# Kernel tuning notes

Hardware: AMD Instinct MI355X
Metric: run time of the kernel (lower is better)

## Reference

```python
import jax, jax.numpy as jnp
import numpy as np

NEG = -1e6  # masked_softmax fill value from the original code


def setup_inputs() -> dict:
    key = jax.random.key(0)
    ks = jax.random.split(key, 8)
    B, Q, K, Dq, Dk, Dv, H = 8, 256, 1024, 256, 256, 128, 128
    queries = jax.random.normal(ks[0], (B, Q, Dq), dtype=jnp.float32)
    keys = jax.random.normal(ks[1], (B, K, Dk), dtype=jnp.float32)
    values = jax.random.normal(ks[2], (B, K, Dv), dtype=jnp.float32)
    valid_lens = jax.random.randint(ks[3], (B,), 1, K + 1, dtype=jnp.int32)
    # learned params (Dense, use_bias=False): y = x @ W
    W_q = jax.random.normal(ks[4], (Dq, H), dtype=jnp.float32) / np.sqrt(Dq)
    W_k = jax.random.normal(ks[5], (Dk, H), dtype=jnp.float32) / np.sqrt(Dk)
    w_v = jax.random.normal(ks[6], (H,), dtype=jnp.float32) / np.sqrt(H)
    return {"queries": queries, "keys": keys, "values": values,
            "valid_lens": valid_lens, "W_q": W_q, "W_k": W_k, "w_v": w_v}


def reference(queries, keys, values, valid_lens, W_q, W_k, w_v):
    q = jnp.einsum('bqd,dh->bqh', queries, W_q)          # [B,Q,H]
    k = jnp.einsum('bkd,dh->bkh', keys, W_k)             # [B,K,H]
    features = jnp.tanh(q[:, :, None, :] + k[:, None, :, :])  # [B,Q,K,H]
    scores = jnp.einsum('bqkh,h->bqk', features, w_v)    # [B,Q,K]
    # masked softmax over last axis: positions >= valid_len set to -1e6
    K_len = scores.shape[-1]
    mask = jnp.arange(K_len)[None, None, :] < valid_lens[:, None, None]
    scores = jnp.where(mask, scores, NEG)
    attn = jax.nn.softmax(scores, axis=-1)
    return jnp.einsum('bqk,bkv->bqv', attn, values)      # [B,Q,Dv]
```

## Files before the change

kernel.cpp:

```cpp
#include <hip/hip_runtime.h>
#include <hip/hip_bf16.h>

#if defined(__has_builtin)
#if __has_builtin(__builtin_amdgcn_exp2f)
#define EXP2F __builtin_amdgcn_exp2f
#endif
#if __has_builtin(__builtin_amdgcn_rcpf)
#define RCPF __builtin_amdgcn_rcpf
#endif
#endif
#ifndef EXP2F
#define EXP2F exp2f
#endif
#ifndef RCPF
#define RCPF(x) (1.0f / (x))
#endif

#define B_  8
#define Q_  256
#define K_  1024
#define D_  256
#define H_  128
#define DV_ 128

#define CSL 2.8853900817779268f
#define L2E 1.4426950408889634f

__global__ __launch_bounds__(256) void proj_kernel(
    const float* __restrict__ queries, const float* __restrict__ keys,
    const float* __restrict__ Wq, const float* __restrict__ Wk,
    float* __restrict__ qE, float* __restrict__ kE)
{
    __shared__ __align__(16) float As[16][36];
    __shared__ __align__(16) float Ws[32][128];

    const int tid = threadIdx.x;
    const int blk = blockIdx.x;
    const bool isQ = blk < 128;
    const int row0 = isQ ? blk * 16 : (blk - 128) * 16;
    const float* A = isQ ? (queries + row0 * D_) : (keys + row0 * D_);
    const float* W = isQ ? Wq : Wk;

    float acc[8];
#pragma unroll
    for (int j = 0; j < 8; j++) acc[j] = 0.f;

    const int r  = tid >> 4;
    const int c8 = (tid & 15) * 8;

    for (int d0 = 0; d0 < D_; d0 += 32) {
        if (tid < 128) {
            const int rr = tid >> 3, cc = (tid & 7) * 4;
            *(float4*)&As[rr][cc] = *(const float4*)&A[rr * D_ + d0 + cc];
        }
#pragma unroll
        for (int l = 0; l < 4; l++) {
            const int idx = tid + l * 256;
            const int rr = idx >> 5, cc = (idx & 31) * 4;
            *(float4*)&Ws[rr][cc] = *(const float4*)&W[(d0 + rr) * H_ + cc];
        }
        __syncthreads();
#pragma unroll
        for (int d = 0; d < 32; d++) {
            const float a = As[r][d];
            const float4 w0 = *(const float4*)&Ws[d][c8];
            const float4 w1 = *(const float4*)&Ws[d][c8 + 4];
            acc[0] = fmaf(a, w0.x, acc[0]);
            acc[1] = fmaf(a, w0.y, acc[1]);
            acc[2] = fmaf(a, w0.z, acc[2]);
            acc[3] = fmaf(a, w0.w, acc[3]);
            acc[4] = fmaf(a, w1.x, acc[4]);
            acc[5] = fmaf(a, w1.y, acc[5]);
            acc[6] = fmaf(a, w1.z, acc[6]);
            acc[7] = fmaf(a, w1.w, acc[7]);
        }
        __syncthreads();
    }

    float e[8];
#pragma unroll
    for (int j = 0; j < 8; j++) e[j] = EXP2F(CSL * acc[j]);

    if (isQ) {
        float* dst = qE + (row0 + r) * H_ + c8;
        *(float4*)dst = make_float4(e[0], e[1], e[2], e[3]);
        *(float4*)(dst + 4) = make_float4(e[4], e[5], e[6], e[7]);
    } else {
        const int krow = row0 + r;
        const int b = krow >> 10, k = krow & 1023;
        float* dst = kE + b * (H_ * K_) + c8 * K_ + k;
#pragma unroll
        for (int j = 0; j < 8; j++) dst[j * K_] = e[j];
    }
}

__global__ __launch_bounds__(512) void attn_kernel(
    const float* __restrict__ qE,
    const float* __restrict__ kE,
    const float* __restrict__ values,
    const int*   __restrict__ valid_lens,
    const float* __restrict__ w_v,
    float* __restrict__ out)
{
    __shared__ __align__(16) float sc[K_][4];
    __shared__ __align__(16) float qs[H_][4];
    __shared__ float wv2[H_];
    __shared__ __align__(16) float psum[8][4];
    __shared__ float rl[4];
    __shared__ __align__(16) float red[16][4][128];

    const int tid = threadIdx.x;
    const int b  = blockIdx.y;
    const int q0 = blockIdx.x * 4;

    if (tid < H_) wv2[tid] = -2.0f * L2E * w_v[tid];
    {
        const float* src = qE + (b * Q_ + q0) * H_;
        const int h = tid & 127, q = tid >> 7;
        qs[h][q] = src[q * H_ + h];
    }
    __syncthreads();

    float a0x = 0.f, a0y = 0.f, a1x = 0.f, a1y = 0.f;
    float a2x = 0.f, a2y = 0.f, a3x = 0.f, a3y = 0.f;
    const int k0 = tid * 2;
    const float* kb = kE + b * (H_ * K_) + k0;
#pragma unroll 4
    for (int h = 0; h < H_; h++) {
        const float2 ek = *(const float2*)(kb + h * K_);
        const float4 qv = *(const float4*)&qs[h][0];
        const float wh = wv2[h];
        float t, r;
        t = fmaf(qv.x, ek.x, 1.0f); r = RCPF(t); a0x = fmaf(wh, r, a0x);
        t = fmaf(qv.x, ek.y, 1.0f); r = RCPF(t); a0y = fmaf(wh, r, a0y);
        t = fmaf(qv.y, ek.x, 1.0f); r = RCPF(t); a1x = fmaf(wh, r, a1x);
        t = fmaf(qv.y, ek.y, 1.0f); r = RCPF(t); a1y = fmaf(wh, r, a1y);
        t = fmaf(qv.z, ek.x, 1.0f); r = RCPF(t); a2x = fmaf(wh, r, a2x);
        t = fmaf(qv.z, ek.y, 1.0f); r = RCPF(t); a2y = fmaf(wh, r, a2y);
        t = fmaf(qv.w, ek.x, 1.0f); r = RCPF(t); a3x = fmaf(wh, r, a3x);
        t = fmaf(qv.w, ek.y, 1.0f); r = RCPF(t); a3y = fmaf(wh, r, a3y);
    }

    const int vl = valid_lens[b];
    float p0x = (k0     < vl) ? EXP2F(a0x) : 0.f;
    float p0y = (k0 + 1 < vl) ? EXP2F(a0y) : 0.f;
    float p1x = (k0     < vl) ? EXP2F(a1x) : 0.f;
    float p1y = (k0 + 1 < vl) ? EXP2F(a1y) : 0.f;
    float p2x = (k0     < vl) ? EXP2F(a2x) : 0.f;
    float p2y = (k0 + 1 < vl) ? EXP2F(a2y) : 0.f;
    float p3x = (k0     < vl) ? EXP2F(a3x) : 0.f;
    float p3y = (k0 + 1 < vl) ? EXP2F(a3y) : 0.f;
    *(float4*)&sc[k0][0]     = make_float4(p0x, p1x, p2x, p3x);
    *(float4*)&sc[k0 + 1][0] = make_float4(p0y, p1y, p2y, p3y);

    float ps[4] = {p0x + p0y, p1x + p1y, p2x + p2y, p3x + p3y};
#pragma unroll
    for (int s = 32; s > 0; s >>= 1) {
#pragma unroll
        for (int q = 0; q < 4; q++) ps[q] += __shfl_xor(ps[q], s);
    }
    const int lane = tid & 63, w = tid >> 6;
    if (lane == 0) *(float4*)&psum[w][0] = make_float4(ps[0], ps[1], ps[2], ps[3]);
    __syncthreads();
    if (tid < 4) {
        float s = 0.f;
#pragma unroll
        for (int ww = 0; ww < 8; ww++) s += psum[ww][tid];
        rl[tid] = RCPF(s);
    }

    {
        const int v4 = (tid & 31) * 4;
        const int kc = tid >> 5;
        const float* vb = values + b * (K_ * DV_) + v4;
        float av[4][4];
#pragma unroll
        for (int q = 0; q < 4; q++)
#pragma unroll
            for (int j = 0; j < 4; j++) av[q][j] = 0.f;
#pragma unroll 2
        for (int kk = 0; kk < 64; kk++) {
            const int k = kc * 64 + kk;
            const float4 vv = *(const float4*)&vb[k * DV_];
            const float4 p  = *(const float4*)&sc[k][0];
            av[0][0] = fmaf(p.x, vv.x, av[0][0]);
            av[0][1] = fmaf(p.x, vv.y, av[0][1]);
            av[0][2] = fmaf(p.x, vv.z, av[0][2]);
            av[0][3] = fmaf(p.x, vv.w, av[0][3]);
            av[1][0] = fmaf(p.y, vv.x, av[1][0]);
            av[1][1] = fmaf(p.y, vv.y, av[1][1]);
            av[1][2] = fmaf(p.y, vv.z, av[1][2]);
            av[1][3] = fmaf(p.y, vv.w, av[1][3]);
            av[2][0] = fmaf(p.z, vv.x, av[2][0]);
            av[2][1] = fmaf(p.z, vv.y, av[2][1]);
            av[2][2] = fmaf(p.z, vv.z, av[2][2]);
            av[2][3] = fmaf(p.z, vv.w, av[2][3]);
            av[3][0] = fmaf(p.w, vv.x, av[3][0]);
            av[3][1] = fmaf(p.w, vv.y, av[3][1]);
            av[3][2] = fmaf(p.w, vv.z, av[3][2]);
            av[3][3] = fmaf(p.w, vv.w, av[3][3]);
        }
#pragma unroll
        for (int q = 0; q < 4; q++)
            *(float4*)&red[kc][q][v4] =
                make_float4(av[q][0], av[q][1], av[q][2], av[q][3]);
    }
    __syncthreads();

    {
        const int q = tid >> 7, v = tid & 127;
        float s = 0.f;
#pragma unroll
        for (int g = 0; g < 16; g++) s += red[g][q][v];
        out[(b * Q_ + q0 + q) * DV_ + v] = s * rl[q];
    }
}

extern "C" void kernel_launch(void* const* d_in, const int* in_sizes, int n_in,
                              void* d_out, int out_size, void* d_ws, size_t ws_size,
                              hipStream_t stream) {
    const float* queries    = (const float*)d_in[0];
    const float* keys       = (const float*)d_in[1];
    const float* values     = (const float*)d_in[2];
    const int*   valid_lens = (const int*)d_in[3];
    const float* W_q        = (const float*)d_in[4];
    const float* W_k        = (const float*)d_in[5];
    const float* w_v        = (const float*)d_in[6];
    float* out = (float*)d_out;

    float* qE = (float*)d_ws;
    float* kE = qE + (B_ * Q_ * H_);

    proj_kernel<<<640, 256, 0, stream>>>(queries, keys, W_q, W_k, qE, kE);
    attn_kernel<<<dim3(Q_ / 4, B_), 512, 0, stream>>>(qE, kE, values, valid_lens, w_v, out);
}
```

Baseline: 145.8 us.

## Pair tanh terms to share one reciprocal, split-K projection, 1024-thread attention

The attention score loop now combines two hidden units per step into a single rational expression, so each pair of tanh terms costs one reciprocal instead of two. The pre-scaled w_v values are precomputed into a packed buffer. The projection becomes a split-D GEMM with larger register tiles, followed by a finish kernel that reduces the partials, applies exp and transposes K through shared memory with coalesced writes. The attention kernel moves to 1024 threads, one key per thread, reading q directly from global memory. This adds kernel launches and workspace traffic for the partials, and the combined formula may behave differently numerically when the exponentials are large.

```diff
diff --git a/kernel.cpp b/kernel.cpp
--- a/kernel.cpp
+++ b/kernel.cpp
@@ -26,7 +26,130 @@
 #define CSL 2.8853900817779268f
 #define L2E 1.4426950408889634f
 
-__global__ __launch_bounds__(256) void proj_kernel(
+#define QE_OFF   0
+#define KE_OFF   262144
+#define WPK_OFF  1310720
+#define PART_OFF 1311744
+#define PSZ      1310720
+
+__global__ __launch_bounds__(256) void proj_split(
+    const float* __restrict__ queries, const float* __restrict__ keys,
+    const float* __restrict__ Wq, const float* __restrict__ Wk,
+    float* __restrict__ part, int nchunk)
+{
+    __shared__ __align__(16) float As[64][68];
+    __shared__ __align__(16) float Ws[64][128];
+
+    const int tid = threadIdx.x;
+    const int rt = blockIdx.x;
+    const bool isQ = rt < 32;
+    const int row0 = isQ ? rt * 64 : (rt - 32) * 64;
+    const int crow0 = isQ ? row0 : row0 + 2048;
+    const float* A = isQ ? (queries + row0 * D_) : (keys + row0 * D_);
+    const float* W = isQ ? Wq : Wk;
+
+    float acc[8][4];
+#pragma unroll
+    for (int i = 0; i < 8; i++)
+#pragma unroll
+        for (int j = 0; j < 4; j++) acc[i][j] = 0.f;
+
+    const int rgrp = tid >> 5;
+    const int c0 = (tid & 31) * 4;
+    const int lr = tid & 63;
+    const int ld = (tid >> 6) * 16;
+
+    for (int ch = 0; ch < nchunk; ch++) {
+        const int d0 = (blockIdx.y * nchunk + ch) * 64;
+#pragma unroll
+        for (int j = 0; j < 4; j++) {
+            const float4 a = *(const float4*)&A[lr * D_ + d0 + ld + j * 4];
+            As[ld + j * 4 + 0][lr] = a.x;
+            As[ld + j * 4 + 1][lr] = a.y;
+            As[ld + j * 4 + 2][lr] = a.z;
+            As[ld + j * 4 + 3][lr] = a.w;
+        }
+#pragma unroll
+        for (int l = 0; l < 8; l++) {
+            const int idx = tid + l * 256;
+            const int rr = idx >> 5, cc = (idx & 31) * 4;
+            *(float4*)&Ws[rr][cc] = *(const float4*)&W[(d0 + rr) * H_ + cc];
+        }
+        __syncthreads();
+#pragma unroll 4
+        for (int d = 0; d < 64; d++) {
+            const float4 w = *(const float4*)&Ws[d][c0];
+            const float4 a0 = *(const float4*)&As[d][rgrp * 8];
+            const float4 a1 = *(const float4*)&As[d][rgrp * 8 + 4];
+            const float ar[8] = {a0.x, a0.y, a0.z, a0.w, a1.x, a1.y, a1.z, a1.w};
+#pragma unroll
+            for (int i = 0; i < 8; i++) {
+                acc[i][0] = fmaf(ar[i], w.x, acc[i][0]);
+                acc[i][1] = fmaf(ar[i], w.y, acc[i][1]);
+                acc[i][2] = fmaf(ar[i], w.z, acc[i][2]);
+                acc[i][3] = fmaf(ar[i], w.w, acc[i][3]);
+            }
+        }
+        __syncthreads();
+    }
+    float* dst = part + (size_t)blockIdx.y * PSZ + (size_t)(crow0 + rgrp * 8) * H_ + c0;
+#pragma unroll
+    for (int i = 0; i < 8; i++)
+        *(float4*)&dst[i * H_] = make_float4(acc[i][0], acc[i][1], acc[i][2], acc[i][3]);
+}
+
+__global__ __launch_bounds__(256) void finish_kernel(
+    const float* __restrict__ part, int S,
+    const float* __restrict__ w_v,
+    float* __restrict__ qE, float* __restrict__ kET, float* __restrict__ wpk)
+{
+    __shared__ float T[128][33];
+    const int tid = threadIdx.x;
+    const int row0 = blockIdx.x * 32;
+    const bool isQ = row0 < 2048;
+
+    float e[16];
+#pragma unroll
+    for (int i = 0; i < 16; i++) {
+        const int idx = row0 * H_ + tid + i * 256;
+        float v = part[idx];
+        for (int s = 1; s < S; s++) v += part[(size_t)s * PSZ + idx];
+        e[i] = EXP2F(CSL * v);
+    }
+    if (isQ) {
+#pragma unroll
+        for (int i = 0; i < 16; i++) qE[row0 * H_ + tid + i * 256] = e[i];
+    } else {
+#pragma unroll
+        for (int i = 0; i < 16; i++) {
+            const int idx = tid + i * 256;
+            T[idx & 127][idx >> 7] = e[i];
+        }
+        __syncthreads();
+        const int krow0 = row0 - 2048;
+        const int b = krow0 >> 10, k0 = krow0 & 1023;
+        const int h = tid >> 1, kh = (tid & 1) * 16;
+        float* dst = kET + (size_t)b * (H_ * K_) + (size_t)h * K_ + k0 + kh;
+#pragma unroll
+        for (int j = 0; j < 4; j++)
+            *(float4*)&dst[j * 4] = make_float4(T[h][kh + j * 4], T[h][kh + j * 4 + 1],
+                                                T[h][kh + j * 4 + 2], T[h][kh + j * 4 + 3]);
+    }
+    if (blockIdx.x == 0 && tid < 64) {
+        const float w1 = -2.0f * L2E * w_v[2 * tid];
+        const float w2 = -2.0f * L2E * w_v[2 * tid + 1];
+        *(float4*)&wpk[tid * 4] = make_float4(w1, w2, w1 + w2, 0.f);
+    }
+}
+
+__global__ void wpk_kernel(const float* __restrict__ w_v, float* __restrict__ wpk) {
+    const int t = threadIdx.x;
+    const float w1 = -2.0f * L2E * w_v[2 * t];
+    const float w2 = -2.0f * L2E * w_v[2 * t + 1];
+    *(float4*)&wpk[t * 4] = make_float4(w1, w2, w1 + w2, 0.f);
+}
+
+__global__ __launch_bounds__(256) void proj_direct(
     const float* __restrict__ queries, const float* __restrict__ keys,
     const float* __restrict__ Wq, const float* __restrict__ Wk,
     float* __restrict__ qE, float* __restrict__ kE)
@@ -44,8 +167,7 @@
     float acc[8];
 #pragma unroll
     for (int j = 0; j < 8; j++) acc[j] = 0.f;
-
-    const int r  = tid >> 4;
+    const int r = tid >> 4;
     const int c8 = (tid & 15) * 8;
 
     for (int d0 = 0; d0 < D_; d0 += 32) {
@@ -65,22 +187,16 @@
             const float a = As[r][d];
             const float4 w0 = *(const float4*)&Ws[d][c8];
             const float4 w1 = *(const float4*)&Ws[d][c8 + 4];
-            acc[0] = fmaf(a, w0.x, acc[0]);
-            acc[1] = fmaf(a, w0.y, acc[1]);
-            acc[2] = fmaf(a, w0.z, acc[2]);
-            acc[3] = fmaf(a, w0.w, acc[3]);
-            acc[4] = fmaf(a, w1.x, acc[4]);
-            acc[5] = fmaf(a, w1.y, acc[5]);
-            acc[6] = fmaf(a, w1.z, acc[6]);
-            acc[7] = fmaf(a, w1.w, acc[7]);
-        }
-        __syncthreads();
-    }
-
+            acc[0] = fmaf(a, w0.x, acc[0]); acc[1] = fmaf(a, w0.y, acc[1]);
+            acc[2] = fmaf(a, w0.z, acc[2]); acc[3] = fmaf(a, w0.w, acc[3]);
+            acc[4] = fmaf(a, w1.x, acc[4]); acc[5] = fmaf(a, w1.y, acc[5]);
+            acc[6] = fmaf(a, w1.z, acc[6]); acc[7] = fmaf(a, w1.w, acc[7]);
+        }
+        __syncthreads();
+    }
     float e[8];
 #pragma unroll
     for (int j = 0; j < 8; j++) e[j] = EXP2F(CSL * acc[j]);
-
     if (isQ) {
         float* dst = qE + (row0 + r) * H_ + c8;
         *(float4*)dst = make_float4(e[0], e[1], e[2], e[3]);
@@ -94,125 +210,130 @@
     }
 }
 
-__global__ __launch_bounds__(512) void attn_kernel(
+__global__ __launch_bounds__(1024, 8) void attn_kernel(
     const float* __restrict__ qE,
-    const float* __restrict__ kE,
+    const float* __restrict__ kET,
     const float* __restrict__ values,
     const int*   __restrict__ valid_lens,
-    const float* __restrict__ w_v,
+    const float* __restrict__ wpk,
     float* __restrict__ out)
 {
     __shared__ __align__(16) float sc[K_][4];
-    __shared__ __align__(16) float qs[H_][4];
-    __shared__ float wv2[H_];
-    __shared__ __align__(16) float psum[8][4];
+    __shared__ __align__(16) float red[16][4][128];
+    __shared__ __align__(16) float psum[16][4];
     __shared__ float rl[4];
-    __shared__ __align__(16) float red[16][4][128];
 
     const int tid = threadIdx.x;
     const int b  = blockIdx.y;
     const int q0 = blockIdx.x * 4;
 
-    if (tid < H_) wv2[tid] = -2.0f * L2E * w_v[tid];
-    {
-        const float* src = qE + (b * Q_ + q0) * H_;
-        const int h = tid & 127, q = tid >> 7;
-        qs[h][q] = src[q * H_ + h];
-    }
-    __syncthreads();
-
-    float a0x = 0.f, a0y = 0.f, a1x = 0.f, a1y = 0.f;
-    float a2x = 0.f, a2y = 0.f, a3x = 0.f, a3y = 0.f;
-    const int k0 = tid * 2;
-    const float* kb = kE + b * (H_ * K_) + k0;
+    const float* q0p = qE + (b * Q_ + q0) * H_;
+    const float* q1p = q0p + H_;
+    const float* q2p = q0p + 2 * H_;
+    const float* q3p = q0p + 3 * H_;
+    const float* kb = kET + (size_t)b * (H_ * K_) + tid;
+
+    float2 acc01 = make_float2(0.f, 0.f);
+    float2 acc23 = make_float2(0.f, 0.f);
+
 #pragma unroll 4
-    for (int h = 0; h < H_; h++) {
-        const float2 ek = *(const float2*)(kb + h * K_);
-        const float4 qv = *(const float4*)&qs[h][0];
-        const float wh = wv2[h];
-        float t, r;
-        t = fmaf(qv.x, ek.x, 1.0f); r = RCPF(t); a0x = fmaf(wh, r, a0x);
-        t = fmaf(qv.x, ek.y, 1.0f); r = RCPF(t); a0y = fmaf(wh, r, a0y);
-        t = fmaf(qv.y, ek.x, 1.0f); r = RCPF(t); a1x = fmaf(wh, r, a1x);
-        t = fmaf(qv.y, ek.y, 1.0f); r = RCPF(t); a1y = fmaf(wh, r, a1y);
-        t = fmaf(qv.z, ek.x, 1.0f); r = RCPF(t); a2x = fmaf(wh, r, a2x);
-        t = fmaf(qv.z, ek.y, 1.0f); r = RCPF(t); a2y = fmaf(wh, r, a2y);
-        t = fmaf(qv.w, ek.x, 1.0f); r = RCPF(t); a3x = fmaf(wh, r, a3x);
-        t = fmaf(qv.w, ek.y, 1.0f); r = RCPF(t); a3y = fmaf(wh, r, a3y);
+    for (int p = 0; p < 64; p++) {
+        const float ek1 = kb[(2 * p) * K_];
+        const float ek2 = kb[(2 * p + 1) * K_];
+        const float4 wp = *(const float4*)&wpk[p * 4];
+        const float2 qa = *(const float2*)&q0p[2 * p];
+        const float2 qb = *(const float2*)&q1p[2 * p];
+        const float2 qc = *(const float2*)&q2p[2 * p];
+        const float2 qd = *(const float2*)&q3p[2 * p];
+        {
+            float2 x1 = make_float2(qa.x * ek1, qb.x * ek1);
+            float2 x2 = make_float2(qa.y * ek2, qb.y * ek2);
+            float2 e1 = make_float2(x1.x + 1.f, x1.y + 1.f);
+            float2 d  = make_float2(fmaf(e1.x, x2.x, e1.x), fmaf(e1.y, x2.y, e1.y));
+            float2 n  = make_float2(fmaf(wp.y, x1.x, wp.z), fmaf(wp.y, x1.y, wp.z));
+            n = make_float2(fmaf(wp.x, x2.x, n.x), fmaf(wp.x, x2.y, n.y));
+            acc01.x = fmaf(n.x, RCPF(d.x), acc01.x);
+            acc01.y = fmaf(n.y, RCPF(d.y), acc01.y);
+        }
+        {
+            float2 x1 = make_float2(qc.x * ek1, qd.x * ek1);
+            float2 x2 = make_float2(qc.y * ek2, qd.y * ek2);
+            float2 e1 = make_float2(x1.x + 1.f, x1.y + 1.f);
+            float2 d  = make_float2(fmaf(e1.x, x2.x, e1.x), fmaf(e1.y, x2.y, e1.y));
+            float2 n  = make_float2(fmaf(wp.y, x1.x, wp.z), fmaf(wp.y, x1.y, wp.z));
+            n = make_float2(fmaf(wp.x, x2.x, n.x), fmaf(wp.x, x2.y, n.y));
+            acc23.x = fmaf(n.x, RCPF(d.x), acc23.x);
+            acc23.y = fmaf(n.y, RCPF(d.y), acc23.y);
+        }
     }
 
     const int vl = valid_lens[b];
-    float p0x = (k0     < vl) ? EXP2F(a0x) : 0.f;
-    float p0y = (k0 + 1 < vl) ? EXP2F(a0y) : 0.f;
-    float p1x = (k0     < vl) ? EXP2F(a1x) : 0.f;
-    float p1y = (k0 + 1 < vl) ? EXP2F(a1y) : 0.f;
-    float p2x = (k0     < vl) ? EXP2F(a2x) : 0.f;
-    float p2y = (k0 + 1 < vl) ? EXP2F(a2y) : 0.f;
-    float p3x = (k0     < vl) ? EXP2F(a3x) : 0.f;
-    float p3y = (k0 + 1 < vl) ? EXP2F(a3y) : 0.f;
-    *(float4*)&sc[k0][0]     = make_float4(p0x, p1x, p2x, p3x);
-    *(float4*)&sc[k0 + 1][0] = make_float4(p0y, p1y, p2y, p3y);
-
-    float ps[4] = {p0x + p0y, p1x + p1y, p2x + p2y, p3x + p3y};
-#pragma unroll
-    for (int s = 32; s > 0; s >>= 1) {
-#pragma unroll
-        for (int q = 0; q < 4; q++) ps[q] += __shfl_xor(ps[q], s);
+    const bool valid = tid < vl;
+    float4 pv;
+    pv.x = valid ? EXP2F(acc01.x) : 0.f;
+    pv.y = valid ? EXP2F(acc01.y) : 0.f;
+    pv.z = valid ? EXP2F(acc23.x) : 0.f;
+    pv.w = valid ? EXP2F(acc23.y) : 0.f;
+    *(float4*)&sc[tid][0] = pv;
+
+    float4 s = pv;
+#pragma unroll
+    for (int sh = 32; sh > 0; sh >>= 1) {
+        s.x += __shfl_xor(s.x, sh);
+        s.y += __shfl_xor(s.y, sh);
+        s.z += __shfl_xor(s.z, sh);
+        s.w += __shfl_xor(s.w, sh);
     }
     const int lane = tid & 63, w = tid >> 6;
-    if (lane == 0) *(float4*)&psum[w][0] = make_float4(ps[0], ps[1], ps[2], ps[3]);
+    if (lane == 0) *(float4*)&psum[w][0] = s;
     __syncthreads();
     if (tid < 4) {
-        float s = 0.f;
-#pragma unroll
-        for (int ww = 0; ww < 8; ww++) s += psum[ww][tid];
-        rl[tid] = RCPF(s);
-    }
-
-    {
-        const int v4 = (tid & 31) * 4;
-        const int kc = tid >> 5;
-        const float* vb = values + b * (K_ * DV_) + v4;
-        float av[4][4];
+        float t = 0.f;
+#pragma unroll
+        for (int ww = 0; ww < 16; ww++) t += psum[ww][tid];
+        rl[tid] = RCPF(t);
+    }
+
+    const int vg = (tid & 31) * 4;
+    const int kh = (tid >> 5) & 1;
+    const int kc = tid >> 6;
+    const float* vb = values + (size_t)b * (K_ * DV_) + vg;
+    float av[4][4];
+#pragma unroll
+    for (int q = 0; q < 4; q++)
+#pragma unroll
+        for (int j = 0; j < 4; j++) av[q][j] = 0.f;
+#pragma unroll 2
+    for (int i = 0; i < 32; i++) {
+        const int k = kc * 64 + i * 2 + kh;
+        const float4 vv = *(const float4*)&vb[k * DV_];
+        const float4 p = *(const float4*)&sc[k][0];
+        av[0][0] = fmaf(p.x, vv.x, av[0][0]); av[0][1] = fmaf(p.x, vv.y, av[0][1]);
+        av[0][2] = fmaf(p.x, vv.z, av[0][2]); av[0][3] = fmaf(p.x, vv.w, av[0][3]);
+        av[1][0] = fmaf(p.y, vv.x, av[1][0]); av[1][1] = fmaf(p.y, vv.y, av[1][1]);
+        av[1][2] = fmaf(p.y, vv.z, av[1][2]); av[1][3] = fmaf(p.y, vv.w, av[1][3]);
+        av[2][0] = fmaf(p.z, vv.x, av[2][0]); av[2][1] = fmaf(p.z, vv.y, av[2][1]);
+        av[2][2] = fmaf(p.z, vv.z, av[2][2]); av[2][3] = fmaf(p.z, vv.w, av[2][3]);
+        av[3][0] = fmaf(p.w, vv.x, av[3][0]); av[3][1] = fmaf(p.w, vv.y, av[3][1]);
+        av[3][2] = fmaf(p.w, vv.z, av[3][2]); av[3][3] = fmaf(p.w, vv.w, av[3][3]);
+    }
+#pragma unroll
+    for (int q = 0; q < 4; q++)
+#pragma unroll
+        for (int j = 0; j < 4; j++) av[q][j] += __shfl_xor(av[q][j], 32);
+    if (kh == 0) {
 #pragma unroll
         for (int q = 0; q < 4; q++)
-#pragma unroll
-            for (int j = 0; j < 4; j++) av[q][j] = 0.f;
-#pragma unroll 2
-        for (int kk = 0; kk < 64; kk++) {
-            const int k = kc * 64 + kk;
-            const float4 vv = *(const float4*)&vb[k * DV_];
-            const float4 p  = *(const float4*)&sc[k][0];
-            av[0][0] = fmaf(p.x, vv.x, av[0][0]);
-            av[0][1] = fmaf(p.x, vv.y, av[0][1]);
-            av[0][2] = fmaf(p.x, vv.z, av[0][2]);
-            av[0][3] = fmaf(p.x, vv.w, av[0][3]);
-            av[1][0] = fmaf(p.y, vv.x, av[1][0]);
-            av[1][1] = fmaf(p.y, vv.y, av[1][1]);
-            av[1][2] = fmaf(p.y, vv.z, av[1][2]);
-            av[1][3] = fmaf(p.y, vv.w, av[1][3]);
-            av[2][0] = fmaf(p.z, vv.x, av[2][0]);
-            av[2][1] = fmaf(p.z, vv.y, av[2][1]);
-            av[2][2] = fmaf(p.z, vv.z, av[2][2]);
-            av[2][3] = fmaf(p.z, vv.w, av[2][3]);
-            av[3][0] = fmaf(p.w, vv.x, av[3][0]);
-            av[3][1] = fmaf(p.w, vv.y, av[3][1]);
-            av[3][2] = fmaf(p.w, vv.z, av[3][2]);
-            av[3][3] = fmaf(p.w, vv.w, av[3][3]);
-        }
-#pragma unroll
-        for (int q = 0; q < 4; q++)
-            *(float4*)&red[kc][q][v4] =
-                make_float4(av[q][0], av[q][1], av[q][2], av[q][3]);
+            *(float4*)&red[kc][q][vg] = make_float4(av[q][0], av[q][1], av[q][2], av[q][3]);
     }
     __syncthreads();
 
-    {
+    if (tid < 512) {
         const int q = tid >> 7, v = tid & 127;
-        float s = 0.f;
-#pragma unroll
-        for (int g = 0; g < 16; g++) s += red[g][q][v];
-        out[(b * Q_ + q0 + q) * DV_ + v] = s * rl[q];
+        float t = 0.f;
+#pragma unroll
+        for (int g = 0; g < 16; g++) t += red[g][q][v];
+        out[(b * Q_ + q0 + q) * DV_ + v] = t * rl[q];
     }
 }
 
@@ -228,9 +349,23 @@
     const float* w_v        = (const float*)d_in[6];
     float* out = (float*)d_out;
 
-    float* qE = (float*)d_ws;
-    float* kE = qE + (B_ * Q_ * H_);
-
-    proj_kernel<<<640, 256, 0, stream>>>(queries, keys, W_q, W_k, qE, kE);
-    attn_kernel<<<dim3(Q_ / 4, B_), 512, 0, stream>>>(qE, kE, values, valid_lens, w_v, out);
-}
+    float* ws  = (float*)d_ws;
+    float* qE  = ws + QE_OFF;
+    float* kET = ws + KE_OFF;
+    float* wpk = ws + WPK_OFF;
+    float* part = ws + PART_OFF;
+
+    int S = 0;
+    if (ws_size >= (size_t)(PART_OFF + 4 * (size_t)PSZ) * 4) S = 4;
+    else if (ws_size >= (size_t)(PART_OFF + 2 * (size_t)PSZ) * 4) S = 2;
+    else if (ws_size >= (size_t)(PART_OFF + 1 * (size_t)PSZ) * 4) S = 1;
+
+    if (S > 0) {
+        proj_split<<<dim3(160, S), 256, 0, stream>>>(queries, keys, W_q, W_k, part, 4 / S);
+        finish_kernel<<<320, 256, 0, stream>>>(part, S, w_v, qE, kET, wpk);
+    } else {
+        proj_direct<<<640, 256, 0, stream>>>(queries, keys, W_q, W_k, qE, kET);
+        wpk_kernel<<<1, 64, 0, stream>>>(w_v, wpk);
+    }
+    attn_kernel<<<dim3(Q_ / 4, B_), 1024, 0, stream>>>(qE, kET, values, valid_lens, wpk, out);
+}
```

Measured after the change: 140.1 us. -3.9%, faster.
